# Kernel tuning notes

Hardware: AMD Instinct MI355X
Metric: run time of the kernel (lower is better)

Reference implementation:

```python
import jax, jax.numpy as jnp
import numpy as np

VOCAB = 32000
EMB = 1024
BLOCK = 2048
B = 4


def setup_inputs() -> dict:
    key = jax.random.key(0)
    ks = jax.random.split(key, 10)
    s = EMB ** -0.5
    return {
        "idx": jax.random.randint(ks[0], (B, BLOCK), 0, VOCAB),
        "targets": jax.random.randint(ks[1], (B, BLOCK), 0, VOCAB),
        "tok_emb": jax.random.normal(ks[2], (VOCAB, EMB), jnp.float32),
        "pos_emb": jax.random.normal(ks[3], (BLOCK, EMB), jnp.float32),
        "Wk": jax.random.normal(ks[4], (EMB, EMB), jnp.float32) * s,
        "Wq": jax.random.normal(ks[5], (EMB, EMB), jnp.float32) * s,
        "Wv": jax.random.normal(ks[6], (EMB, EMB), jnp.float32) * s,
        "Wlm": jax.random.normal(ks[7], (EMB, VOCAB), jnp.float32) * s,
        "blm": jnp.zeros((VOCAB,), jnp.float32),
    }


def reference(idx, targets, tok_emb, pos_emb, Wk, Wq, Wv, Wlm, blm):
    B_, T = idx.shape
    x = tok_emb[idx] + pos_emb[:T]  # [B,T,C]
    C = x.shape[-1]
    k = x @ Wk  # [B,T,H]
    q = x @ Wq
    v = x @ Wv
    wei = jnp.einsum("bth,bsh->bts", q, k) * (C ** -0.5)  # [B,T,T]
    causal = jnp.tril(jnp.ones((T, T), bool))
    wei = jnp.where(causal, wei, -jnp.inf)
    wei = jax.nn.softmax(wei, axis=-1)
    out = jnp.einsum("bts,bsh->bth", wei, v)  # [B,T,H]
    logits = out @ Wlm + blm  # [B,T,V]
    logits2d = logits.reshape(B_ * T, -1)
    tgt = targets.reshape(B_ * T)
    logp = jax.nn.log_softmax(logits2d, axis=-1)
    loss = -jnp.mean(jnp.take_along_axis(logp, tgt[:, None], axis=1))
    return logits2d, loss
```

## Files before the change

kernel.cpp:

```cpp
#include <hip/hip_runtime.h>
#include <hip/hip_bf16.h>
#include <cstdint>

#define VOCAB 32000
#define EMB   1024
#define TLEN  2048
#define NB    4
#define MTOT  (NB*TLEN)

typedef __bf16 bf16;
typedef __bf16 bf16x8 __attribute__((ext_vector_type(8)));
typedef float  f32x4  __attribute__((ext_vector_type(4)));

__global__ void embed_kernel(const int* __restrict__ idx,
                             const float* __restrict__ tok,
                             const float* __restrict__ pos,
                             bf16* __restrict__ x)
{
    int gid = blockIdx.x * 256 + threadIdx.x;
    int r   = gid >> 7;
    int c0  = (gid & 127) << 3;
    int t   = r & (TLEN - 1);
    int tk  = idx[r];
    const float4* tp = reinterpret_cast<const float4*>(tok + (long)tk * EMB + c0);
    const float4* pp = reinterpret_cast<const float4*>(pos + (long)t  * EMB + c0);
    float4 a0 = tp[0], a1 = tp[1];
    float4 b0 = pp[0], b1 = pp[1];
    bf16x8 o;
    o[0] = (bf16)(a0.x + b0.x); o[1] = (bf16)(a0.y + b0.y);
    o[2] = (bf16)(a0.z + b0.z); o[3] = (bf16)(a0.w + b0.w);
    o[4] = (bf16)(a1.x + b1.x); o[5] = (bf16)(a1.y + b1.y);
    o[6] = (bf16)(a1.z + b1.z); o[7] = (bf16)(a1.w + b1.w);
    *reinterpret_cast<bf16x8*>(x + (long)r * EMB + c0) = o;
}

__global__ void transpose_conv_kernel(const float* __restrict__ W,
                                      bf16* __restrict__ Wt,
                                      int Kdim, int Ndim)
{
    __shared__ bf16 tile[64][65];
    int n0 = blockIdx.x * 64;
    int k0 = blockIdx.y * 64;
    int tid = threadIdx.x;
    int c  = tid & 63, r0 = tid >> 6;
#pragma unroll
    for (int i = 0; i < 16; ++i) {
        int r = r0 + i * 4;
        tile[r][c] = (bf16)W[(long)(k0 + r) * Ndim + n0 + c];
    }
    __syncthreads();
    int kc = tid & 63, nr0 = tid >> 6;
#pragma unroll
    for (int i = 0; i < 16; ++i) {
        int nr = nr0 + i * 4;
        Wt[(long)(n0 + nr) * Kdim + k0 + kc] = tile[kc][nr];
    }
}

__device__ __forceinline__ void gll16(const void* g, void* l)
{
    __builtin_amdgcn_global_load_lds(
        (const __attribute__((address_space(1))) unsigned int*)g,
        (__attribute__((address_space(3))) unsigned int*)l, 16, 0, 0);
}

template<int OMODE, int CMODE>
__global__ __launch_bounds__(256)
void gemm_bt_kernel(const bf16* __restrict__ A, int lda, long sA,
                    const bf16* __restrict__ Bt, int ldb, long sB,
                    void* __restrict__ Cv, int ldc, long sC,
                    int K, const float* __restrict__ bias)
{
    if (CMODE == 1 && blockIdx.x > blockIdx.y) return;

    __shared__ bf16 As[128 * 32];
    __shared__ bf16 Bs[128 * 32];

    const int tid  = threadIdx.x;
    const int lane = tid & 63;
    const int wv   = tid >> 6;
    const int wr   = wv >> 1, wc = wv & 1;
    const int l15  = lane & 15, hi = lane >> 4;
    const long zb  = blockIdx.z;

    const bf16* Ab = A  + zb * sA + (long)(blockIdx.y * 128) * lda;
    const bf16* Bb = Bt + zb * sB + (long)(blockIdx.x * 128) * ldb;

    const int Keff = (CMODE == 2) ? (int)((blockIdx.y + 1) * 128) : K;

    f32x4 acc[4][4] = {};

    const int l0 = tid, l1 = tid + 256;
    const int r0s = l0 >> 2, kg0 = ((l0 & 3) ^ ((r0s >> 1) & 3)) * 8;
    const int r1s = l1 >> 2, kg1 = ((l1 & 3) ^ ((r1s >> 1) & 3)) * 8;

    for (int kt = 0; kt < Keff; kt += 32) {
        if (kt) __syncthreads();
        gll16(Ab + (long)r0s * lda + kt + kg0, &As[l0 * 8]);
        gll16(Ab + (long)r1s * lda + kt + kg1, &As[l1 * 8]);
        gll16(Bb + (long)r0s * ldb + kt + kg0, &Bs[l0 * 8]);
        gll16(Bb + (long)r1s * ldb + kt + kg1, &Bs[l1 * 8]);
        __syncthreads();

        const int kos = (hi ^ ((l15 >> 1) & 3)) * 8;
        bf16x8 af[4], bfr[4];
#pragma unroll
        for (int i = 0; i < 4; ++i) {
            af[i]  = *reinterpret_cast<const bf16x8*>(
                         &As[(wr * 64 + i * 16 + l15) * 32 + kos]);
            bfr[i] = *reinterpret_cast<const bf16x8*>(
                         &Bs[(wc * 64 + i * 16 + l15) * 32 + kos]);
        }
#pragma unroll
        for (int i = 0; i < 4; ++i)
#pragma unroll
            for (int j = 0; j < 4; ++j)
                acc[i][j] = __builtin_amdgcn_mfma_f32_16x16x32_bf16(
                                af[i], bfr[j], acc[i][j], 0, 0, 0);
    }

    const int rowb = blockIdx.y * 128 + wr * 64 + (hi << 2);
    const int colb = blockIdx.x * 128 + wc * 64 + l15;

    if (OMODE == 0) {
        bf16* C = (bf16*)Cv + zb * sC;
#pragma unroll
        for (int i = 0; i < 4; ++i)
#pragma unroll
            for (int j = 0; j < 4; ++j)
#pragma unroll
                for (int r = 0; r < 4; ++r)
                    C[(long)(rowb + i * 16 + r) * ldc + colb + j * 16] = (bf16)acc[i][j][r];
    } else {
        float* C = (float*)Cv + zb * sC;
#pragma unroll
        for (int i = 0; i < 4; ++i)
#pragma unroll
            for (int j = 0; j < 4; ++j)
#pragma unroll
                for (int r = 0; r < 4; ++r)
                    C[(long)(rowb + i * 16 + r) * ldc + colb + j * 16] = acc[i][j][r];
    }
}

__device__ __forceinline__ void stage256(const bf16* __restrict__ gbase, int kt,
                                         bf16* lbase, int tid)
{
#pragma unroll
    for (int p = 0; p < 4; ++p) {
        int lin  = p * 512 + tid;
        int row  = lin >> 3;
        int slot = lin & 7;
        int ke   = ((slot ^ (row & 7)) << 3) + kt;
        gll16(gbase + (long)row * EMB + ke, lbase + lin * 8);
    }
}

__global__ __launch_bounds__(512)
void gemm256_logits(const bf16* __restrict__ A, const bf16* __restrict__ Bt,
                    float* __restrict__ C, const float* __restrict__ bias,
                    float2* __restrict__ part)
{
    extern __shared__ bf16 smem[];
    bf16* As = smem;
    bf16* Bs = smem + 32768;

    const int tid  = threadIdx.x;
    const int lane = tid & 63, wid = tid >> 6;
    const int wr = wid >> 2, wc = wid & 3;
    const int l15 = lane & 15, hi = lane >> 4, l7 = lane & 7;

    const int wg = blockIdx.x;
    const int xcd = wg & 7, c = wg >> 3;
    const int nb = c >> 2;
    const int mb = xcd * 4 + (c & 3);

    const bf16* Ab = A  + (long)(mb * 256) * EMB;
    const bf16* Bb = Bt + (long)(nb * 256) * EMB;

    f32x4 acc[8][4] = {};

    stage256(Ab, 0, As, tid);
    stage256(Bb, 0, Bs, tid);
    __syncthreads();

    const int NT = EMB / 64;
    for (int t = 0; t < NT; ++t) {
        const int buf = t & 1;
        if (t + 1 < NT) {
            stage256(Ab, (t + 1) * 64, As + (buf ^ 1) * 16384, tid);
            stage256(Bb, (t + 1) * 64, Bs + (buf ^ 1) * 16384, tid);
        }
        const bf16* Ap = As + buf * 16384 + (wr * 128) * 64;
        const bf16* Bp = Bs + buf * 16384 + (wc * 64) * 64;
#pragma unroll
        for (int ks = 0; ks < 2; ++ks) {
            const int ko = 8 * (((ks << 2) | hi) ^ l7);
            bf16x8 bfr[4];
#pragma unroll
            for (int n = 0; n < 4; ++n)
                bfr[n] = *(const bf16x8*)(Bp + (n * 16 + l15) * 64 + ko);
#pragma unroll
            for (int m = 0; m < 8; ++m) {
                bf16x8 af = *(const bf16x8*)(Ap + (m * 16 + l15) * 64 + ko);
#pragma unroll
                for (int n = 0; n < 4; ++n)
                    acc[m][n] = __builtin_amdgcn_mfma_f32_16x16x32_bf16(
                                    af, bfr[n], acc[m][n], 0, 0, 0);
            }
        }
        __syncthreads();
    }

    float* pm = (float*)smem;
    float* ps = pm + 1024;

    const long colbase = (long)nb * 256 + wc * 64 + l15;
    float bv[4];
#pragma unroll
    for (int n = 0; n < 4; ++n) bv[n] = bias[colbase + n * 16];

    const long rowbase = (long)mb * 256 + wr * 128;
#pragma unroll
    for (int m = 0; m < 8; ++m) {
#pragma unroll
        for (int r = 0; r < 4; ++r) {
            float v0 = acc[m][0][r] + bv[0];
            float v1 = acc[m][1][r] + bv[1];
            float v2 = acc[m][2][r] + bv[2];
            float v3 = acc[m][3][r] + bv[3];
            long row = rowbase + m * 16 + (hi << 2) + r;
            float* Cp = C + row * (long)VOCAB + colbase;
            Cp[0] = v0; Cp[16] = v1; Cp[32] = v2; Cp[48] = v3;

            float lm = fmaxf(fmaxf(v0, v1), fmaxf(v2, v3));
#pragma unroll
            for (int o = 1; o < 16; o <<= 1) lm = fmaxf(lm, __shfl_xor(lm, o));
            float sp = __expf(v0 - lm) + __expf(v1 - lm) +
                       __expf(v2 - lm) + __expf(v3 - lm);
#pragma unroll
            for (int o = 1; o < 16; o <<= 1) sp += __shfl_xor(sp, o);
            if (l15 == 0) {
                int rb = wr * 128 + m * 16 + (hi << 2) + r;
                pm[wc * 256 + rb] = lm;
                ps[wc * 256 + rb] = sp;
            }
        }
    }
    __syncthreads();
    if (tid < 256) {
        float m0 = pm[tid], m1 = pm[256 + tid], m2 = pm[512 + tid], m3 = pm[768 + tid];
        float M = fmaxf(fmaxf(m0, m1), fmaxf(m2, m3));
        float S = ps[tid] * __expf(m0 - M) + ps[256 + tid] * __expf(m1 - M) +
                  ps[512 + tid] * __expf(m2 - M) + ps[768 + tid] * __expf(m3 - M);
        part[((long)mb * 256 + tid) * 125 + nb] = make_float2(M, S);
    }
}

__global__ void softmax_causal_kernel(const bf16* __restrict__ S,
                                      bf16* __restrict__ P)
{
    const int r = blockIdx.x;
    const int t = r & (TLEN - 1);
    const int limit = ((t >> 7) + 1) << 7;
    const int tid = threadIdx.x;
    const int lane = tid & 63, wv = tid >> 6;
    const float scale = 0.03125f;
    const int c0 = tid * 8;

    float v[8];
    float m = -1e30f;
    if (c0 < limit) {
        bf16x8 sv = *(const bf16x8*)(S + (long)r * TLEN + c0);
#pragma unroll
        for (int i = 0; i < 8; ++i) {
            float x = (c0 + i <= t) ? (float)sv[i] * scale : -1e30f;
            v[i] = x;
            m = fmaxf(m, x);
        }
    } else {
#pragma unroll
        for (int i = 0; i < 8; ++i) v[i] = -1e30f;
    }
    __shared__ float red[4];
#pragma unroll
    for (int off = 32; off; off >>= 1) m = fmaxf(m, __shfl_xor(m, off));
    if (lane == 0) red[wv] = m;
    __syncthreads();
    m = fmaxf(fmaxf(red[0], red[1]), fmaxf(red[2], red[3]));
    __syncthreads();

    float s = 0.f;
#pragma unroll
    for (int i = 0; i < 8; ++i) { v[i] = __expf(v[i] - m); s += v[i]; }
#pragma unroll
    for (int off = 32; off; off >>= 1) s += __shfl_xor(s, off);
    if (lane == 0) red[wv] = s;
    __syncthreads();
    s = red[0] + red[1] + red[2] + red[3];
    float inv = 1.0f / s;
    if (c0 < limit) {
        bf16x8 o;
#pragma unroll
        for (int i = 0; i < 8; ++i) o[i] = (bf16)(v[i] * inv);
        *(bf16x8*)(P + (long)r * TLEN + c0) = o;
    }
}

__global__ void loss_combine_kernel(const float2* __restrict__ part,
                                    const float* __restrict__ logits,
                                    const int* __restrict__ tgt,
                                    float* __restrict__ bsum)
{
    const int tid = threadIdx.x;
    const int row = blockIdx.x * 256 + tid;
    const int lane = tid & 63, wv = tid >> 6;
    const float2* p = part + (long)row * 125;
    float M = -1e30f, S = 0.f;
    for (int i = 0; i < 125; ++i) {
        float2 v = p[i];
        if (v.x <= M) S += v.y * __expf(v.x - M);
        else { S = S * __expf(M - v.x) + v.y; M = v.x; }
    }
    float lse = M + __logf(S);
    float l = lse - logits[(long)row * VOCAB + tgt[row]];
#pragma unroll
    for (int off = 32; off; off >>= 1) l += __shfl_xor(l, off);
    __shared__ float red[4];
    if (lane == 0) red[wv] = l;
    __syncthreads();
    if (tid == 0) bsum[blockIdx.x] = red[0] + red[1] + red[2] + red[3];
}

__global__ void loss_final_kernel(const float* __restrict__ bsum,
                                  float* __restrict__ out)
{
    const int lane = threadIdx.x;
    float s = (lane < 32) ? bsum[lane] : 0.f;
#pragma unroll
    for (int off = 32; off; off >>= 1) s += __shfl_xor(s, off);
    if (lane == 0) out[0] = s * (1.0f / MTOT);
}

extern "C" void kernel_launch(void* const* d_in, const int* in_sizes, int n_in,
                              void* d_out, int out_size, void* d_ws, size_t ws_size,
                              hipStream_t stream)
{
    const int*   idx = (const int*)  d_in[0];
    const int*   tgt = (const int*)  d_in[1];
    const float* tok = (const float*)d_in[2];
    const float* pos = (const float*)d_in[3];
    const float* Wk  = (const float*)d_in[4];
    const float* Wq  = (const float*)d_in[5];
    const float* Wv  = (const float*)d_in[6];
    const float* Wlm = (const float*)d_in[7];
    const float* blm = (const float*)d_in[8];
    float* out = (float*)d_out;

    char* ws = (char*)d_ws;
    if (ws_size < (size_t)140 * 1024 * 1024) return;

    bf16*   x     = (bf16*)(ws);
    bf16*   qk    = (bf16*)(ws + (16l << 20));
    bf16*   v_t   = (bf16*)(ws + (48l << 20));
    bf16*   S     = (bf16*)(ws + (64l << 20));
    bf16*   Wqk_t = (bf16*)(ws + (96l << 20));
    bf16*   Wv_t  = (bf16*)(ws + (100l << 20));
    bf16*   att   = (bf16*)(ws);
    bf16*   P     = (bf16*)(ws + (16l << 20));
    bf16*   Wlm_t = (bf16*)(ws + (48l << 20));
    float2* part  = (float2*)(ws + (112l << 20));
    float*  bsum  = (float*)(ws + (120l << 20));

    embed_kernel<<<dim3(MTOT * EMB / 8 / 256), 256, 0, stream>>>(idx, tok, pos, x);

    transpose_conv_kernel<<<dim3(16, 16), 256, 0, stream>>>(Wq, Wqk_t, EMB, EMB);
    transpose_conv_kernel<<<dim3(16, 16), 256, 0, stream>>>(Wk, Wqk_t + 1024 * 1024, EMB, EMB);
    transpose_conv_kernel<<<dim3(16, 16), 256, 0, stream>>>(Wv, Wv_t, EMB, EMB);

    gemm_bt_kernel<0,0><<<dim3(2048 / 128, MTOT / 128, 1), 256, 0, stream>>>(
        x, EMB, 0, Wqk_t, EMB, 0, qk, 2048, 0, EMB, nullptr);
    gemm_bt_kernel<0,0><<<dim3(MTOT / 128, EMB / 128, 1), 256, 0, stream>>>(
        Wv_t, EMB, 0, x, EMB, 0, v_t, MTOT, 0, EMB, nullptr);

    gemm_bt_kernel<0,1><<<dim3(TLEN / 128, TLEN / 128, NB), 256, 0, stream>>>(
        qk, 2048, (long)TLEN * 2048, qk + 1024, 2048, (long)TLEN * 2048,
        S, TLEN, (long)TLEN * TLEN, EMB, nullptr);

    softmax_causal_kernel<<<dim3(MTOT), 256, 0, stream>>>(S, P);

    gemm_bt_kernel<0,2><<<dim3(EMB / 128, TLEN / 128, NB), 256, 0, stream>>>(
        P, TLEN, (long)TLEN * TLEN, v_t, MTOT, (long)TLEN,
        att, EMB, (long)TLEN * EMB, TLEN, nullptr);

    transpose_conv_kernel<<<dim3(VOCAB / 64, EMB / 64), 256, 0, stream>>>(
        Wlm, Wlm_t, EMB, VOCAB);

    gemm256_logits<<<dim3(4000), 512, 131072, stream>>>(att, Wlm_t, out, blm, part);

    loss_combine_kernel<<<dim3(32), 256, 0, stream>>>(part, out, tgt, bsum);
    loss_final_kernel<<<dim3(1), 64, 0, stream>>>(bsum, out + (long)MTOT * VOCAB);
}
```

Baseline: 952.0 us.

## Software-pipeline logits GEMM with triple-buffered B and fine-grained barrier phases

Restructures the main loop of the 256x256 logits GEMM into four sub-phases per K-tile. Each phase loads A/B fragments from LDS, issues global-to-LDS staging for the next tiles, and runs a quarter of the MFMAs at raised wave priority, with explicit waitcnt and barrier control. B gets a third LDS buffer and is prefetched two tiles ahead, so dynamic shared memory grows from 128 KiB to 160 KiB. The aim is to overlap memory staging with MFMA work and cut stalls at the single full barrier. The cost is more barriers per tile, hand-tuned vmcnt counts that depend on stage256's load count, and higher LDS use.

New measurement: 967.2 us. About the same (+1.6%).

```diff
diff --git a/kernel.cpp b/kernel.cpp
--- a/kernel.cpp
+++ b/kernel.cpp
@@ -180,37 +180,83 @@
 
     f32x4 acc[8][4] = {};
 
-    stage256(Ab, 0, As, tid);
-    stage256(Bb, 0, Bs, tid);
-    __syncthreads();
-
-    const int NT = EMB / 64;
-    for (int t = 0; t < NT; ++t) {
-        const int buf = t & 1;
-        if (t + 1 < NT) {
-            stage256(Ab, (t + 1) * 64, As + (buf ^ 1) * 16384, tid);
-            stage256(Bb, (t + 1) * 64, Bs + (buf ^ 1) * 16384, tid);
+    const int ko0 = 8 * (hi ^ l7);
+    const int ko1 = 8 * ((4 | hi) ^ l7);
+    const bf16* ApR = As + (wr * 128 + l15) * 64;
+    const bf16* BpR = Bs + (wc * 64  + l15) * 64;
+
+#define LGKM0 do { asm volatile("s_waitcnt lgkmcnt(0)" ::: "memory");        \
+                   __builtin_amdgcn_sched_barrier(0); } while (0)
+#define MFMA_Q(mbase)                                                        \
+    __builtin_amdgcn_s_setprio(1);                                           \
+    _Pragma("unroll")                                                        \
+    for (int m_ = 0; m_ < 4; ++m_)                                           \
+        _Pragma("unroll")                                                    \
+        for (int n_ = 0; n_ < 4; ++n_)                                       \
+            acc[(mbase) + m_][n_] = __builtin_amdgcn_mfma_f32_16x16x32_bf16( \
+                af[m_], bfr[n_], acc[(mbase) + m_][n_], 0, 0, 0);            \
+    __builtin_amdgcn_s_setprio(0);
+
+    stage256(Ab, 0,  As, tid);
+    stage256(Bb, 0,  Bs, tid);
+    stage256(Bb, 64, Bs + 16384, tid);
+    asm volatile("s_waitcnt vmcnt(4)" ::: "memory");
+    __builtin_amdgcn_sched_barrier(0);
+    __builtin_amdgcn_s_barrier();
+
+    int bB = 0;
+#pragma unroll 1
+    for (int t = 0; t < 16; ++t) {
+        const bf16* Ap = ApR + (t & 1) * 16384;
+        const bf16* Bp = BpR + bB * 16384;
+        int b2 = bB + 2; if (b2 >= 3) b2 -= 3;
+        bf16x8 af[4], bfr[4];
+
+#pragma unroll
+        for (int n = 0; n < 4; ++n) bfr[n] = *(const bf16x8*)(Bp + n * 1024 + ko0);
+#pragma unroll
+        for (int m = 0; m < 4; ++m) af[m]  = *(const bf16x8*)(Ap + m * 1024 + ko0);
+        if (t < 15) stage256(Ab, (t + 1) * 64, As + ((t & 1) ^ 1) * 16384, tid);
+        __builtin_amdgcn_s_barrier();
+        LGKM0;
+        MFMA_Q(0);
+        __builtin_amdgcn_s_barrier();
+
+#pragma unroll
+        for (int m = 0; m < 4; ++m) af[m] = *(const bf16x8*)(Ap + (4 + m) * 1024 + ko0);
+        if (t < 14) stage256(Bb, (t + 2) * 64, Bs + b2 * 16384, tid);
+        __builtin_amdgcn_s_barrier();
+        LGKM0;
+        MFMA_Q(4);
+        __builtin_amdgcn_s_barrier();
+
+#pragma unroll
+        for (int n = 0; n < 4; ++n) bfr[n] = *(const bf16x8*)(Bp + n * 1024 + ko1);
+#pragma unroll
+        for (int m = 0; m < 4; ++m) af[m]  = *(const bf16x8*)(Ap + m * 1024 + ko1);
+        __builtin_amdgcn_s_barrier();
+        LGKM0;
+        MFMA_Q(0);
+        __builtin_amdgcn_s_barrier();
+
+#pragma unroll
+        for (int m = 0; m < 4; ++m) af[m] = *(const bf16x8*)(Ap + (4 + m) * 1024 + ko1);
+        __builtin_amdgcn_s_barrier();
+        LGKM0;
+        MFMA_Q(4);
+        if (t < 14) {
+            asm volatile("s_waitcnt vmcnt(4)" ::: "memory");
+            __builtin_amdgcn_sched_barrier(0);
+        } else if (t == 14) {
+            asm volatile("s_waitcnt vmcnt(0)" ::: "memory");
+            __builtin_amdgcn_sched_barrier(0);
         }
-        const bf16* Ap = As + buf * 16384 + (wr * 128) * 64;
-        const bf16* Bp = Bs + buf * 16384 + (wc * 64) * 64;
-#pragma unroll
-        for (int ks = 0; ks < 2; ++ks) {
-            const int ko = 8 * (((ks << 2) | hi) ^ l7);
-            bf16x8 bfr[4];
-#pragma unroll
-            for (int n = 0; n < 4; ++n)
-                bfr[n] = *(const bf16x8*)(Bp + (n * 16 + l15) * 64 + ko);
-#pragma unroll
-            for (int m = 0; m < 8; ++m) {
-                bf16x8 af = *(const bf16x8*)(Ap + (m * 16 + l15) * 64 + ko);
-#pragma unroll
-                for (int n = 0; n < 4; ++n)
-                    acc[m][n] = __builtin_amdgcn_mfma_f32_16x16x32_bf16(
-                                    af, bfr[n], acc[m][n], 0, 0, 0);
-            }
-        }
-        __syncthreads();
-    }
+        __builtin_amdgcn_s_barrier();
+
+        bB = (bB == 2) ? 0 : bB + 1;
+    }
+#undef MFMA_Q
+#undef LGKM0
 
     float* pm = (float*)smem;
     float* ps = pm + 1024;
@@ -396,7 +442,7 @@
     transpose_conv_kernel<<<dim3(VOCAB / 64, EMB / 64), 256, 0, stream>>>(
         Wlm, Wlm_t, EMB, VOCAB);
 
-    gemm256_logits<<<dim3(4000), 512, 131072, stream>>>(att, Wlm_t, out, blm, part);
+    gemm256_logits<<<dim3(4000), 512, 163840, stream>>>(att, Wlm_t, out, blm, part);
 
     loss_combine_kernel<<<dim3(32), 256, 0, stream>>>(part, out, tgt, bsum);
     loss_final_kernel<<<dim3(1), 64, 0, stream>>>(bsum, out + (long)MTOT * VOCAB);
```

## Replace 128-tile attention GEMMs with double-buffered 256-tile kernel; nontemporal logits stores

Applied to the files above, without the earlier changes.

Swaps the small 128x128 single-buffered GEMM used for the QKV projections, QK^T and PV products for a generalized 256x256, 512-thread, double-buffered LDS kernel taken from the logits GEMM. Causal skipping and the softmax valid-column limit move to 256 granularity to match the new tiles. Logits stores become nontemporal to avoid polluting cache. Larger tiles raise reuse but give fewer blocks for the small GEMMs, and coarser causal granularity does some extra masked work.

Result: faster. 847.2 us (-11.0%).

```diff
diff --git a/kernel.cpp b/kernel.cpp
--- a/kernel.cpp
+++ b/kernel.cpp
@@ -64,87 +64,8 @@
         (__attribute__((address_space(3))) unsigned int*)l, 16, 0, 0);
 }
 
-template<int OMODE, int CMODE>
-__global__ __launch_bounds__(256)
-void gemm_bt_kernel(const bf16* __restrict__ A, int lda, long sA,
-                    const bf16* __restrict__ Bt, int ldb, long sB,
-                    void* __restrict__ Cv, int ldc, long sC,
-                    int K, const float* __restrict__ bias)
-{
-    if (CMODE == 1 && blockIdx.x > blockIdx.y) return;
-
-    __shared__ bf16 As[128 * 32];
-    __shared__ bf16 Bs[128 * 32];
-
-    const int tid  = threadIdx.x;
-    const int lane = tid & 63;
-    const int wv   = tid >> 6;
-    const int wr   = wv >> 1, wc = wv & 1;
-    const int l15  = lane & 15, hi = lane >> 4;
-    const long zb  = blockIdx.z;
-
-    const bf16* Ab = A  + zb * sA + (long)(blockIdx.y * 128) * lda;
-    const bf16* Bb = Bt + zb * sB + (long)(blockIdx.x * 128) * ldb;
-
-    const int Keff = (CMODE == 2) ? (int)((blockIdx.y + 1) * 128) : K;
-
-    f32x4 acc[4][4] = {};
-
-    const int l0 = tid, l1 = tid + 256;
-    const int r0s = l0 >> 2, kg0 = ((l0 & 3) ^ ((r0s >> 1) & 3)) * 8;
-    const int r1s = l1 >> 2, kg1 = ((l1 & 3) ^ ((r1s >> 1) & 3)) * 8;
-
-    for (int kt = 0; kt < Keff; kt += 32) {
-        if (kt) __syncthreads();
-        gll16(Ab + (long)r0s * lda + kt + kg0, &As[l0 * 8]);
-        gll16(Ab + (long)r1s * lda + kt + kg1, &As[l1 * 8]);
-        gll16(Bb + (long)r0s * ldb + kt + kg0, &Bs[l0 * 8]);
-        gll16(Bb + (long)r1s * ldb + kt + kg1, &Bs[l1 * 8]);
-        __syncthreads();
-
-        const int kos = (hi ^ ((l15 >> 1) & 3)) * 8;
-        bf16x8 af[4], bfr[4];
-#pragma unroll
-        for (int i = 0; i < 4; ++i) {
-            af[i]  = *reinterpret_cast<const bf16x8*>(
-                         &As[(wr * 64 + i * 16 + l15) * 32 + kos]);
-            bfr[i] = *reinterpret_cast<const bf16x8*>(
-                         &Bs[(wc * 64 + i * 16 + l15) * 32 + kos]);
-        }
-#pragma unroll
-        for (int i = 0; i < 4; ++i)
-#pragma unroll
-            for (int j = 0; j < 4; ++j)
-                acc[i][j] = __builtin_amdgcn_mfma_f32_16x16x32_bf16(
-                                af[i], bfr[j], acc[i][j], 0, 0, 0);
-    }
-
-    const int rowb = blockIdx.y * 128 + wr * 64 + (hi << 2);
-    const int colb = blockIdx.x * 128 + wc * 64 + l15;
-
-    if (OMODE == 0) {
-        bf16* C = (bf16*)Cv + zb * sC;
-#pragma unroll
-        for (int i = 0; i < 4; ++i)
-#pragma unroll
-            for (int j = 0; j < 4; ++j)
-#pragma unroll
-                for (int r = 0; r < 4; ++r)
-                    C[(long)(rowb + i * 16 + r) * ldc + colb + j * 16] = (bf16)acc[i][j][r];
-    } else {
-        float* C = (float*)Cv + zb * sC;
-#pragma unroll
-        for (int i = 0; i < 4; ++i)
-#pragma unroll
-            for (int j = 0; j < 4; ++j)
-#pragma unroll
-                for (int r = 0; r < 4; ++r)
-                    C[(long)(rowb + i * 16 + r) * ldc + colb + j * 16] = acc[i][j][r];
-    }
-}
-
-__device__ __forceinline__ void stage256(const bf16* __restrict__ gbase, int kt,
-                                         bf16* lbase, int tid)
+__device__ __forceinline__ void stage256s(const bf16* __restrict__ gbase,
+                                          int ld, int kt, bf16* lbase, int tid)
 {
 #pragma unroll
     for (int p = 0; p < 4; ++p) {
@@ -152,8 +73,79 @@
         int row  = lin >> 3;
         int slot = lin & 7;
         int ke   = ((slot ^ (row & 7)) << 3) + kt;
-        gll16(gbase + (long)row * EMB + ke, lbase + lin * 8);
-    }
+        gll16(gbase + (long)row * ld + ke, lbase + lin * 8);
+    }
+}
+
+template<int CMODE>
+__global__ __launch_bounds__(512)
+void gemm256_bt(const bf16* __restrict__ A, int lda, long sA,
+                const bf16* __restrict__ Bt, int ldb, long sB,
+                bf16* __restrict__ C, int ldc, long sC, int K)
+{
+    if (CMODE == 1 && blockIdx.x > blockIdx.y) return;
+
+    extern __shared__ bf16 smem[];
+    bf16* As = smem;
+    bf16* Bs = smem + 32768;
+
+    const int tid  = threadIdx.x;
+    const int lane = tid & 63, wid = tid >> 6;
+    const int wr = wid >> 2, wc = wid & 3;
+    const int l15 = lane & 15, hi = lane >> 4, l7 = lane & 7;
+    const long zb = blockIdx.z;
+
+    const bf16* Ab = A  + zb * sA + (long)(blockIdx.y * 256) * lda;
+    const bf16* Bb = Bt + zb * sB + (long)(blockIdx.x * 256) * ldb;
+
+    const int Keff = (CMODE == 2) ? (int)((blockIdx.y + 1) * 256) : K;
+    const int NT   = Keff >> 6;
+
+    f32x4 acc[8][4] = {};
+
+    stage256s(Ab, lda, 0, As, tid);
+    stage256s(Bb, ldb, 0, Bs, tid);
+    __syncthreads();
+
+#pragma unroll 1
+    for (int t = 0; t < NT; ++t) {
+        const int buf = t & 1;
+        if (t + 1 < NT) {
+            stage256s(Ab, lda, (t + 1) * 64, As + (buf ^ 1) * 16384, tid);
+            stage256s(Bb, ldb, (t + 1) * 64, Bs + (buf ^ 1) * 16384, tid);
+        }
+        const bf16* Ap = As + buf * 16384 + (wr * 128) * 64;
+        const bf16* Bp = Bs + buf * 16384 + (wc * 64) * 64;
+#pragma unroll
+        for (int ks = 0; ks < 2; ++ks) {
+            const int ko = 8 * (((ks << 2) | hi) ^ l7);
+            bf16x8 bfr[4];
+#pragma unroll
+            for (int n = 0; n < 4; ++n)
+                bfr[n] = *(const bf16x8*)(Bp + (n * 16 + l15) * 64 + ko);
+#pragma unroll
+            for (int m = 0; m < 8; ++m) {
+                bf16x8 af = *(const bf16x8*)(Ap + (m * 16 + l15) * 64 + ko);
+#pragma unroll
+                for (int n = 0; n < 4; ++n)
+                    acc[m][n] = __builtin_amdgcn_mfma_f32_16x16x32_bf16(
+                                    af, bfr[n], acc[m][n], 0, 0, 0);
+            }
+        }
+        __syncthreads();
+    }
+
+    bf16* Cb = C + zb * sC;
+    const int colb = blockIdx.x * 256 + wc * 64 + l15;
+    const int rowb = blockIdx.y * 256 + wr * 128 + (hi << 2);
+#pragma unroll
+    for (int m = 0; m < 8; ++m)
+#pragma unroll
+        for (int n = 0; n < 4; ++n)
+#pragma unroll
+            for (int r = 0; r < 4; ++r)
+                Cb[(long)(rowb + m * 16 + r) * ldc + colb + n * 16] =
+                    (bf16)acc[m][n][r];
 }
 
 __global__ __launch_bounds__(512)
@@ -180,16 +172,17 @@
 
     f32x4 acc[8][4] = {};
 
-    stage256(Ab, 0, As, tid);
-    stage256(Bb, 0, Bs, tid);
+    stage256s(Ab, EMB, 0, As, tid);
+    stage256s(Bb, EMB, 0, Bs, tid);
     __syncthreads();
 
     const int NT = EMB / 64;
+#pragma unroll 1
     for (int t = 0; t < NT; ++t) {
         const int buf = t & 1;
         if (t + 1 < NT) {
-            stage256(Ab, (t + 1) * 64, As + (buf ^ 1) * 16384, tid);
-            stage256(Bb, (t + 1) * 64, Bs + (buf ^ 1) * 16384, tid);
+            stage256s(Ab, EMB, (t + 1) * 64, As + (buf ^ 1) * 16384, tid);
+            stage256s(Bb, EMB, (t + 1) * 64, Bs + (buf ^ 1) * 16384, tid);
         }
         const bf16* Ap = As + buf * 16384 + (wr * 128) * 64;
         const bf16* Bp = Bs + buf * 16384 + (wc * 64) * 64;
@@ -231,7 +224,10 @@
             float v3 = acc[m][3][r] + bv[3];
             long row = rowbase + m * 16 + (hi << 2) + r;
             float* Cp = C + row * (long)VOCAB + colbase;
-            Cp[0] = v0; Cp[16] = v1; Cp[32] = v2; Cp[48] = v3;
+            __builtin_nontemporal_store(v0, Cp);
+            __builtin_nontemporal_store(v1, Cp + 16);
+            __builtin_nontemporal_store(v2, Cp + 32);
+            __builtin_nontemporal_store(v3, Cp + 48);
 
             float lm = fmaxf(fmaxf(v0, v1), fmaxf(v2, v3));
 #pragma unroll
@@ -262,7 +258,7 @@
 {
     const int r = blockIdx.x;
     const int t = r & (TLEN - 1);
-    const int limit = ((t >> 7) + 1) << 7;
+    const int limit = ((t >> 8) + 1) << 8;
     const int tid = threadIdx.x;
     const int lane = tid & 63, wv = tid >> 6;
     const float scale = 0.03125f;
@@ -378,20 +374,20 @@
     transpose_conv_kernel<<<dim3(16, 16), 256, 0, stream>>>(Wk, Wqk_t + 1024 * 1024, EMB, EMB);
     transpose_conv_kernel<<<dim3(16, 16), 256, 0, stream>>>(Wv, Wv_t, EMB, EMB);
 
-    gemm_bt_kernel<0,0><<<dim3(2048 / 128, MTOT / 128, 1), 256, 0, stream>>>(
-        x, EMB, 0, Wqk_t, EMB, 0, qk, 2048, 0, EMB, nullptr);
-    gemm_bt_kernel<0,0><<<dim3(MTOT / 128, EMB / 128, 1), 256, 0, stream>>>(
-        Wv_t, EMB, 0, x, EMB, 0, v_t, MTOT, 0, EMB, nullptr);
-
-    gemm_bt_kernel<0,1><<<dim3(TLEN / 128, TLEN / 128, NB), 256, 0, stream>>>(
+    gemm256_bt<0><<<dim3(2048 / 256, MTOT / 256, 1), 512, 131072, stream>>>(
+        x, EMB, 0, Wqk_t, EMB, 0, qk, 2048, 0, EMB);
+    gemm256_bt<0><<<dim3(MTOT / 256, EMB / 256, 1), 512, 131072, stream>>>(
+        Wv_t, EMB, 0, x, EMB, 0, v_t, MTOT, 0, EMB);
+
+    gemm256_bt<1><<<dim3(TLEN / 256, TLEN / 256, NB), 512, 131072, stream>>>(
         qk, 2048, (long)TLEN * 2048, qk + 1024, 2048, (long)TLEN * 2048,
-        S, TLEN, (long)TLEN * TLEN, EMB, nullptr);
+        S, TLEN, (long)TLEN * TLEN, EMB);
 
     softmax_causal_kernel<<<dim3(MTOT), 256, 0, stream>>>(S, P);
 
-    gemm_bt_kernel<0,2><<<dim3(EMB / 128, TLEN / 128, NB), 256, 0, stream>>>(
+    gemm256_bt<2><<<dim3(EMB / 256, TLEN / 256, NB), 512, 131072, stream>>>(
         P, TLEN, (long)TLEN * TLEN, v_t, MTOT, (long)TLEN,
-        att, EMB, (long)TLEN * EMB, TLEN, nullptr);
+        att, EMB, (long)TLEN * EMB, TLEN);
 
     transpose_conv_kernel<<<dim3(VOCAB / 64, EMB / 64), 256, 0, stream>>>(
         Wlm, Wlm_t, EMB, VOCAB);
```
